# Kernel tuning notes

Measured on AMD Instinct MI355X. Metric: run time of the kernel, lower is better.

The kernel has to match this reference:

```python
import jax, jax.numpy as jnp
import numpy as np

N, E = 20000, 320000
HID, EDIM, DDIM, TDIM = 256, 128, 64, 256
IN_CH = 2 * HID + EDIM + DDIM  # 704
COORS_EPS = 1e-8
LN_EPS = 1e-6


def setup_inputs() -> dict:
    key = jax.random.key(0)
    ks = jax.random.split(key, 16)
    s = lambda fan_in: 1.0 / np.sqrt(fan_in)
    return {
        'h': jax.random.normal(ks[0], (N, HID), jnp.float32),
        'pos': jax.random.normal(ks[1], (N, 3), jnp.float32),
        'edge_attr': jax.random.normal(ks[2], (E, EDIM), jnp.float32),
        'dist': jax.random.uniform(ks[3], (E, DDIM), jnp.float32),
        'time_emb': jax.random.normal(ks[4], (E, TDIM), jnp.float32),
        'edge_index': jax.random.randint(ks[5], (2, E), 0, N, jnp.int64),
        'W_time': jax.random.uniform(ks[6], (TDIM, 2 * HID), jnp.float32, -s(TDIM), s(TDIM)),
        'b_time': jnp.zeros((2 * HID,), jnp.float32),
        'W_in': jax.random.uniform(ks[7], (IN_CH, HID), jnp.float32, -s(IN_CH), s(IN_CH)),
        'b_in': jnp.zeros((HID,), jnp.float32),
        'W_c1': jax.random.uniform(ks[8], (HID, HID), jnp.float32, -s(HID), s(HID)),
        'b_c1': jnp.zeros((HID,), jnp.float32),
        'W_c2': jax.random.uniform(ks[9], (HID, 1), jnp.float32, -s(HID), s(HID)),
        'coord_scale': jnp.full((1,), 0.01, jnp.float32),
    }


def _layernorm_noaffine(x):
    # fp32 LayerNorm, no affine (matches LayerNorm(elementwise_affine=False))
    x32 = x.astype(jnp.float32)
    mu = jnp.mean(x32, axis=-1, keepdims=True)
    var = jnp.mean(jnp.square(x32 - mu), axis=-1, keepdims=True)
    return ((x32 - mu) * jax.lax.rsqrt(var + LN_EPS)).astype(x.dtype)


def reference(h, pos, edge_attr, dist, time_emb, edge_index,
              W_time, b_time, W_in, b_in, W_c1, b_c1, W_c2, coord_scale):
    row, col = edge_index[0], edge_index[1]
    # gather node features per edge: [E, 2*HID + EDIM + DDIM]
    h_input = jnp.concatenate([h[row], h[col], edge_attr, dist], axis=1)
    # equivariant direction, normalized (CoorsNorm)
    coord_diff = pos[row] - pos[col]                       # [E, 3]
    norm = jnp.linalg.norm(coord_diff, axis=-1, keepdims=True)
    coord_diff = coord_diff / jnp.maximum(norm, COORS_EPS) * coord_scale
    # time conditioning: SiLU -> Linear -> chunk to shift/scale [E, HID]
    t = jax.nn.silu(time_emb) @ W_time + b_time
    shift, scale = t[:, :HID], t[:, HID:]
    inv = _layernorm_noaffine(h_input @ W_in + b_in)
    inv = inv * (1.0 + scale) + shift                      # modulate
    # coord MLP -> tanh gate [E, 1]
    inv = jnp.tanh(jax.nn.silu(inv @ W_c1 + b_c1) @ W_c2)
    trans = coord_diff * inv                               # [E, 3]
    agg = jax.ops.segment_sum(trans, row, num_segments=pos.shape[0])
    return pos + agg
```

## Files before the change

kernel.cpp:

```cpp
#include <hip/hip_runtime.h>
#include <hip/hip_bf16.h>

#define NN   20000
#define NE   320000
#define HID  256
#define EDIM 128
#define DDIM 64
#define TDIM 256
#define INCH 704

typedef __attribute__((ext_vector_type(8))) short bf16x8;
typedef __attribute__((ext_vector_type(4))) float f32x4;
typedef __attribute__((ext_vector_type(4))) unsigned int u32x4;

__device__ __forceinline__ unsigned short f2bu(float x) {
    return __bfloat16_as_ushort(__float2bfloat16(x));
}
__device__ __forceinline__ unsigned pk2(float lo, float hi) {
    return (unsigned)f2bu(lo) | ((unsigned)f2bu(hi) << 16);
}
__device__ __forceinline__ float ulo(unsigned u) {
    return __bfloat162float(__ushort_as_bfloat16((unsigned short)(u & 0xffffu)));
}
__device__ __forceinline__ float uhi(unsigned u) {
    return __bfloat162float(__ushort_as_bfloat16((unsigned short)(u >> 16)));
}
__device__ __forceinline__ float silu_f(float x) {
    return x / (1.0f + __expf(-x));
}

__global__ void pack_weights(const float* __restrict__ src, unsigned short* __restrict__ dst,
                             int K, int Nc) {
    int KT = K >> 5, NT = Nc >> 4;
    int total = KT * NT * 64;
    int idx = blockIdx.x * blockDim.x + threadIdx.x;
    if (idx >= total) return;
    int lane = idx & 63;
    int tile = idx >> 6;
    int nt = tile % NT, kt = tile / NT;
    int n = nt * 16 + (lane & 15);
    int k0 = kt * 32 + (lane >> 4) * 8;
    alignas(16) unsigned short v[8];
#pragma unroll
    for (int j = 0; j < 8; ++j) v[j] = f2bu(src[(size_t)(k0 + j) * Nc + n]);
    *reinterpret_cast<u32x4*>(dst + (size_t)idx * 8) = *reinterpret_cast<const u32x4*>(v);
}

__global__ void init_out(const float* __restrict__ pos, float* __restrict__ out, int n) {
    int i = blockIdx.x * blockDim.x + threadIdx.x;
    if (i < n) out[i] = pos[i];
}

__global__ __launch_bounds__(256, 2) void edge_kernel(
    const float* __restrict__ h, const float* __restrict__ pos,
    const float* __restrict__ edge_attr, const float* __restrict__ dist,
    const float* __restrict__ time_emb, const int* __restrict__ edge_index,
    const float* __restrict__ b_time, const float* __restrict__ b_in,
    const float* __restrict__ b_c1, const float* __restrict__ W_c2,
    const float* __restrict__ coord_scale,
    const unsigned short* __restrict__ pWtime, const unsigned short* __restrict__ pWin,
    const unsigned short* __restrict__ pWc1,
    float* __restrict__ out)
{
    __shared__ __align__(16) __hip_bfloat16 sX[2][64][40];
    __shared__ __align__(16) __hip_bfloat16 sU[64][264];
    __shared__ float sSum[64], sSq[64], sS[64];
    __shared__ int sRow[64], sCol[64];

    const int tid = threadIdx.x;
    const int wave = tid >> 6, lane = tid & 63;
    const int lq = lane >> 4, lr = lane & 15;
    const int e0 = blockIdx.x * 64;
    const int el = tid >> 2, part = tid & 3;

    if (tid < 64) {
        sRow[tid] = edge_index[e0 + tid];
        sCol[tid] = edge_index[NE + e0 + tid];
        sSum[tid] = 0.f; sSq[tid] = 0.f; sS[tid] = 0.f;
    }

    auto stageT = [&](int kt, int buf) {
        const float* p = time_emb + (size_t)(e0 + el) * TDIM + kt * 32 + part * 8;
        float4 a = *reinterpret_cast<const float4*>(p);
        float4 b = *reinterpret_cast<const float4*>(p + 4);
        u32x4 w;
        w.x = pk2(silu_f(a.x), silu_f(a.y));
        w.y = pk2(silu_f(a.z), silu_f(a.w));
        w.z = pk2(silu_f(b.x), silu_f(b.y));
        w.w = pk2(silu_f(b.z), silu_f(b.w));
        *reinterpret_cast<u32x4*>(&sX[buf][el][part * 8]) = w;
    };

    f32x4 accT[4][8];
#pragma unroll
    for (int m = 0; m < 4; ++m)
#pragma unroll
        for (int n = 0; n < 8; ++n) accT[m][n] = (f32x4){0.f, 0.f, 0.f, 0.f};

    stageT(0, 0);
    for (int kt = 0; kt < 8; ++kt) {
        __syncthreads();
        if (kt < 7) stageT(kt + 1, (kt + 1) & 1);
        bf16x8 afr[4];
#pragma unroll
        for (int m = 0; m < 4; ++m)
            afr[m] = *reinterpret_cast<const bf16x8*>(&sX[kt & 1][m * 16 + lr][lq * 8]);
#pragma unroll
        for (int n = 0; n < 8; ++n) {
            int ntg = (n < 4) ? (4 * wave + n) : (16 + 4 * wave + (n - 4));
            bf16x8 bfr = *reinterpret_cast<const bf16x8*>(pWtime + ((size_t)(kt * 32 + ntg) * 64 + lane) * 8);
#pragma unroll
            for (int m = 0; m < 4; ++m)
                accT[m][n] = __builtin_amdgcn_mfma_f32_16x16x32_bf16(afr[m], bfr, accT[m][n], 0, 0, 0);
        }
    }

    unsigned TP[4][8][2];
#pragma unroll
    for (int n = 0; n < 8; ++n) {
        int colg = (n < 4) ? ((4 * wave + n) * 16 + lr) : (256 + (4 * wave + (n - 4)) * 16 + lr);
        float bt = b_time[colg];
#pragma unroll
        for (int m = 0; m < 4; ++m) {
            f32x4 v = accT[m][n];
            TP[m][n][0] = pk2(v.x + bt, v.y + bt);
            TP[m][n][1] = pk2(v.z + bt, v.w + bt);
        }
    }

    auto stage1 = [&](int kt, int buf) {
        const float* p;
        if (kt < 8)       p = h + (size_t)sRow[el] * HID + kt * 32;
        else if (kt < 16) p = h + (size_t)sCol[el] * HID + (kt - 8) * 32;
        else if (kt < 20) p = edge_attr + (size_t)(e0 + el) * EDIM + (kt - 16) * 32;
        else              p = dist + (size_t)(e0 + el) * DDIM + (kt - 20) * 32;
        p += part * 8;
        float4 a = *reinterpret_cast<const float4*>(p);
        float4 b = *reinterpret_cast<const float4*>(p + 4);
        u32x4 w;
        w.x = pk2(a.x, a.y); w.y = pk2(a.z, a.w);
        w.z = pk2(b.x, b.y); w.w = pk2(b.z, b.w);
        *reinterpret_cast<u32x4*>(&sX[buf][el][part * 8]) = w;
    };

    f32x4 accY[4][4];
#pragma unroll
    for (int m = 0; m < 4; ++m)
#pragma unroll
        for (int n = 0; n < 4; ++n) accY[m][n] = (f32x4){0.f, 0.f, 0.f, 0.f};

    stage1(0, 0);
    for (int kt = 0; kt < 22; ++kt) {
        __syncthreads();
        if (kt < 21) stage1(kt + 1, (kt + 1) & 1);
        bf16x8 afr[4];
#pragma unroll
        for (int m = 0; m < 4; ++m)
            afr[m] = *reinterpret_cast<const bf16x8*>(&sX[kt & 1][m * 16 + lr][lq * 8]);
#pragma unroll
        for (int n = 0; n < 4; ++n) {
            int ntg = 4 * wave + n;
            bf16x8 bfr = *reinterpret_cast<const bf16x8*>(pWin + ((size_t)(kt * 16 + ntg) * 64 + lane) * 8);
#pragma unroll
            for (int m = 0; m < 4; ++m)
                accY[m][n] = __builtin_amdgcn_mfma_f32_16x16x32_bf16(afr[m], bfr, accY[m][n], 0, 0, 0);
        }
    }

#pragma unroll
    for (int n = 0; n < 4; ++n) {
        float bi = b_in[(4 * wave + n) * 16 + lr];
#pragma unroll
        for (int m = 0; m < 4; ++m) {
            accY[m][n].x += bi; accY[m][n].y += bi; accY[m][n].z += bi; accY[m][n].w += bi;
        }
    }

#pragma unroll
    for (int m = 0; m < 4; ++m) {
#pragma unroll
        for (int r = 0; r < 4; ++r) {
            float v0 = accY[m][0][r], v1 = accY[m][1][r], v2 = accY[m][2][r], v3 = accY[m][3][r];
            float s1 = v0 + v1 + v2 + v3;
            float s2 = v0 * v0 + v1 * v1 + v2 * v2 + v3 * v3;
#pragma unroll
            for (int off = 1; off < 16; off <<= 1) {
                s1 += __shfl_xor(s1, off, 64);
                s2 += __shfl_xor(s2, off, 64);
            }
            if (lr == 0) {
                atomicAdd(&sSum[m * 16 + lq * 4 + r], s1);
                atomicAdd(&sSq[m * 16 + lq * 4 + r], s2);
            }
        }
    }
    __syncthreads();

#pragma unroll
    for (int m = 0; m < 4; ++m) {
#pragma unroll
        for (int r = 0; r < 4; ++r) {
            int e = m * 16 + lq * 4 + r;
            float mu = sSum[e] * (1.0f / 256.0f);
            float var = sSq[e] * (1.0f / 256.0f) - mu * mu;
            float rs = rsqrtf(var + 1e-6f);
#pragma unroll
            for (int n = 0; n < 4; ++n) {
                float y = accY[m][n][r];
                float ln = (y - mu) * rs;
                unsigned ush = TP[m][n][r >> 1];
                unsigned usc = TP[m][n + 4][r >> 1];
                float sh = (r & 1) ? uhi(ush) : ulo(ush);
                float sc = (r & 1) ? uhi(usc) : ulo(usc);
                float u = ln * (1.0f + sc) + sh;
                sU[e][(4 * wave + n) * 16 + lr] = __float2bfloat16(u);
            }
        }
    }
    __syncthreads();

    f32x4 accZ[4][4];
#pragma unroll
    for (int m = 0; m < 4; ++m)
#pragma unroll
        for (int n = 0; n < 4; ++n) accZ[m][n] = (f32x4){0.f, 0.f, 0.f, 0.f};

    for (int kt = 0; kt < 8; ++kt) {
        bf16x8 afr[4];
#pragma unroll
        for (int m = 0; m < 4; ++m)
            afr[m] = *reinterpret_cast<const bf16x8*>(&sU[m * 16 + lr][kt * 32 + lq * 8]);
#pragma unroll
        for (int n = 0; n < 4; ++n) {
            int ntg = 4 * wave + n;
            bf16x8 bfr = *reinterpret_cast<const bf16x8*>(pWc1 + ((size_t)(kt * 16 + ntg) * 64 + lane) * 8);
#pragma unroll
            for (int m = 0; m < 4; ++m)
                accZ[m][n] = __builtin_amdgcn_mfma_f32_16x16x32_bf16(afr[m], bfr, accZ[m][n], 0, 0, 0);
        }
    }

#pragma unroll
    for (int m = 0; m < 4; ++m) {
        float ps0 = 0.f, ps1 = 0.f, ps2 = 0.f, ps3 = 0.f;
#pragma unroll
        for (int n = 0; n < 4; ++n) {
            int colg = (4 * wave + n) * 16 + lr;
            float bc = b_c1[colg];
            float w2 = W_c2[colg];
            ps0 += silu_f(accZ[m][n][0] + bc) * w2;
            ps1 += silu_f(accZ[m][n][1] + bc) * w2;
            ps2 += silu_f(accZ[m][n][2] + bc) * w2;
            ps3 += silu_f(accZ[m][n][3] + bc) * w2;
        }
        float ps[4] = {ps0, ps1, ps2, ps3};
#pragma unroll
        for (int r = 0; r < 4; ++r) {
            float v = ps[r];
#pragma unroll
            for (int off = 1; off < 16; off <<= 1) v += __shfl_xor(v, off, 64);
            if (lr == 0) atomicAdd(&sS[m * 16 + lq * 4 + r], v);
        }
    }
    __syncthreads();

    if (tid < 64) {
        int e = tid;
        float inv = tanhf(sS[e]);
        int rI = sRow[e], cI = sCol[e];
        float dx = pos[rI * 3 + 0] - pos[cI * 3 + 0];
        float dy = pos[rI * 3 + 1] - pos[cI * 3 + 1];
        float dz = pos[rI * 3 + 2] - pos[cI * 3 + 2];
        float nrm = sqrtf(dx * dx + dy * dy + dz * dz);
        float f = coord_scale[0] * inv / fmaxf(nrm, 1e-8f);
        atomicAdd(&out[rI * 3 + 0], dx * f);
        atomicAdd(&out[rI * 3 + 1], dy * f);
        atomicAdd(&out[rI * 3 + 2], dz * f);
    }
}

extern "C" void kernel_launch(void* const* d_in, const int* in_sizes, int n_in,
                              void* d_out, int out_size, void* d_ws, size_t ws_size,
                              hipStream_t stream) {
    const float* h          = (const float*)d_in[0];
    const float* pos        = (const float*)d_in[1];
    const float* edge_attr  = (const float*)d_in[2];
    const float* dist       = (const float*)d_in[3];
    const float* time_emb   = (const float*)d_in[4];
    const int*   edge_index = (const int*)d_in[5];
    const float* W_time     = (const float*)d_in[6];
    const float* b_time     = (const float*)d_in[7];
    const float* W_in       = (const float*)d_in[8];
    const float* b_in       = (const float*)d_in[9];
    const float* W_c1       = (const float*)d_in[10];
    const float* b_c1       = (const float*)d_in[11];
    const float* W_c2       = (const float*)d_in[12];
    const float* coord_scale= (const float*)d_in[13];
    float* out = (float*)d_out;

    unsigned short* pWin   = (unsigned short*)d_ws;
    unsigned short* pWtime = (unsigned short*)((char*)d_ws + 360448);
    unsigned short* pWc1   = (unsigned short*)((char*)d_ws + 622592);

    pack_weights<<<88, 256, 0, stream>>>(W_in,   pWin,   INCH, HID);
    pack_weights<<<64, 256, 0, stream>>>(W_time, pWtime, TDIM, 2 * HID);
    pack_weights<<<32, 256, 0, stream>>>(W_c1,   pWc1,   HID,  HID);
    init_out<<<(3 * NN + 255) / 256, 256, 0, stream>>>(pos, out, 3 * NN);

    edge_kernel<<<NE / 64, 256, 0, stream>>>(
        h, pos, edge_attr, dist, time_emb, edge_index,
        b_time, b_in, b_c1, W_c2, coord_scale,
        pWtime, pWin, pWc1, out);
}
```

Baseline: 552.4 us.

## Restructure edge kernel staging and split time GEMM to raise occupancy

The time-embedding tile is now staged once into a shared buffer, and the time GEMM is computed in two halves (shift, then scale) so only 16 accumulators are live at a time. That buffer is aliased with the U and X tiles to cut shared memory. The input GEMM now uses 64-wide K chunks with register prefetch of the next chunk, which halves the number of barriers. Launch bounds move from 2 to 3 blocks per SIMD so more waves can hide the gather latency, at the risk of register spills.

```diff
diff --git a/kernel.cpp b/kernel.cpp
--- a/kernel.cpp
+++ b/kernel.cpp
@@ -51,7 +51,7 @@
     if (i < n) out[i] = pos[i];
 }
 
-__global__ __launch_bounds__(256, 2) void edge_kernel(
+__global__ __launch_bounds__(256, 3) void edge_kernel(
     const float* __restrict__ h, const float* __restrict__ pos,
     const float* __restrict__ edge_attr, const float* __restrict__ dist,
     const float* __restrict__ time_emb, const int* __restrict__ edge_index,
@@ -62,8 +62,10 @@
     const unsigned short* __restrict__ pWc1,
     float* __restrict__ out)
 {
-    __shared__ __align__(16) __hip_bfloat16 sX[2][64][40];
-    __shared__ __align__(16) __hip_bfloat16 sU[64][264];
+    __shared__ __align__(16) unsigned char smem[64 * 264 * 2];
+    __hip_bfloat16 (*sT)[264]    = reinterpret_cast<__hip_bfloat16(*)[264]>(smem);
+    __hip_bfloat16 (*sU)[264]    = reinterpret_cast<__hip_bfloat16(*)[264]>(smem);
+    __hip_bfloat16 (*sX)[64][72] = reinterpret_cast<__hip_bfloat16(*)[64][72]>(smem);
     __shared__ float sSum[64], sSq[64], sS[64];
     __shared__ int sRow[64], sCol[64];
 
@@ -79,92 +81,156 @@
         sSum[tid] = 0.f; sSq[tid] = 0.f; sS[tid] = 0.f;
     }
 
-    auto stageT = [&](int kt, int buf) {
-        const float* p = time_emb + (size_t)(e0 + el) * TDIM + kt * 32 + part * 8;
-        float4 a = *reinterpret_cast<const float4*>(p);
-        float4 b = *reinterpret_cast<const float4*>(p + 4);
-        u32x4 w;
-        w.x = pk2(silu_f(a.x), silu_f(a.y));
-        w.y = pk2(silu_f(a.z), silu_f(a.w));
-        w.z = pk2(silu_f(b.x), silu_f(b.y));
-        w.w = pk2(silu_f(b.z), silu_f(b.w));
-        *reinterpret_cast<u32x4*>(&sX[buf][el][part * 8]) = w;
-    };
-
-    f32x4 accT[4][8];
+    {
+        const float* p = time_emb + (size_t)(e0 + el) * TDIM + part * 64;
+#pragma unroll
+        for (int j = 0; j < 4; ++j) {
+            float4 a = *reinterpret_cast<const float4*>(p + j * 16);
+            float4 b = *reinterpret_cast<const float4*>(p + j * 16 + 4);
+            float4 c = *reinterpret_cast<const float4*>(p + j * 16 + 8);
+            float4 d = *reinterpret_cast<const float4*>(p + j * 16 + 12);
+            u32x4 w0, w1;
+            w0.x = pk2(silu_f(a.x), silu_f(a.y)); w0.y = pk2(silu_f(a.z), silu_f(a.w));
+            w0.z = pk2(silu_f(b.x), silu_f(b.y)); w0.w = pk2(silu_f(b.z), silu_f(b.w));
+            w1.x = pk2(silu_f(c.x), silu_f(c.y)); w1.y = pk2(silu_f(c.z), silu_f(c.w));
+            w1.z = pk2(silu_f(d.x), silu_f(d.y)); w1.w = pk2(silu_f(d.z), silu_f(d.w));
+            *reinterpret_cast<u32x4*>(&sT[el][part * 64 + j * 16]) = w0;
+            *reinterpret_cast<u32x4*>(&sT[el][part * 64 + j * 16 + 8]) = w1;
+        }
+    }
+    __syncthreads();
+
+    const int rIdx = sRow[el], cIdx = sCol[el];
+
+    float rY[16];
+    {
+        const float* p = h + (size_t)rIdx * HID + part * 16;
+        *reinterpret_cast<float4*>(&rY[0])  = *reinterpret_cast<const float4*>(p);
+        *reinterpret_cast<float4*>(&rY[4])  = *reinterpret_cast<const float4*>(p + 4);
+        *reinterpret_cast<float4*>(&rY[8])  = *reinterpret_cast<const float4*>(p + 8);
+        *reinterpret_cast<float4*>(&rY[12]) = *reinterpret_cast<const float4*>(p + 12);
+    }
+
+    unsigned TPs[4][4][2], TPc[4][4][2];
+    {
+        f32x4 acc[4][4];
+#pragma unroll
+        for (int m = 0; m < 4; ++m)
+#pragma unroll
+            for (int n = 0; n < 4; ++n) acc[m][n] = (f32x4){0.f, 0.f, 0.f, 0.f};
+#pragma unroll
+        for (int kt = 0; kt < 8; ++kt) {
+            bf16x8 afr[4];
+#pragma unroll
+            for (int m = 0; m < 4; ++m)
+                afr[m] = *reinterpret_cast<const bf16x8*>(&sT[m * 16 + lr][kt * 32 + lq * 8]);
+#pragma unroll
+            for (int n = 0; n < 4; ++n) {
+                bf16x8 bfr = *reinterpret_cast<const bf16x8*>(
+                    pWtime + ((size_t)(kt * 32 + 4 * wave + n) * 64 + lane) * 8);
+#pragma unroll
+                for (int m = 0; m < 4; ++m)
+                    acc[m][n] = __builtin_amdgcn_mfma_f32_16x16x32_bf16(afr[m], bfr, acc[m][n], 0, 0, 0);
+            }
+        }
+#pragma unroll
+        for (int n = 0; n < 4; ++n) {
+            float bt = b_time[(4 * wave + n) * 16 + lr];
+#pragma unroll
+            for (int m = 0; m < 4; ++m) {
+                TPs[m][n][0] = pk2(acc[m][n].x + bt, acc[m][n].y + bt);
+                TPs[m][n][1] = pk2(acc[m][n].z + bt, acc[m][n].w + bt);
+            }
+        }
+#pragma unroll
+        for (int m = 0; m < 4; ++m)
+#pragma unroll
+            for (int n = 0; n < 4; ++n) acc[m][n] = (f32x4){0.f, 0.f, 0.f, 0.f};
+#pragma unroll
+        for (int kt = 0; kt < 8; ++kt) {
+            bf16x8 afr[4];
+#pragma unroll
+            for (int m = 0; m < 4; ++m)
+                afr[m] = *reinterpret_cast<const bf16x8*>(&sT[m * 16 + lr][kt * 32 + lq * 8]);
+#pragma unroll
+            for (int n = 0; n < 4; ++n) {
+                bf16x8 bfr = *reinterpret_cast<const bf16x8*>(
+                    pWtime + ((size_t)(kt * 32 + 16 + 4 * wave + n) * 64 + lane) * 8);
+#pragma unroll
+                for (int m = 0; m < 4; ++m)
+                    acc[m][n] = __builtin_amdgcn_mfma_f32_16x16x32_bf16(afr[m], bfr, acc[m][n], 0, 0, 0);
+            }
+        }
+#pragma unroll
+        for (int n = 0; n < 4; ++n) {
+            float bt = b_time[256 + (4 * wave + n) * 16 + lr];
+#pragma unroll
+            for (int m = 0; m < 4; ++m) {
+                TPc[m][n][0] = pk2(acc[m][n].x + bt, acc[m][n].y + bt);
+                TPc[m][n][1] = pk2(acc[m][n].z + bt, acc[m][n].w + bt);
+            }
+        }
+    }
+    __syncthreads();
+
+    {
+        u32x4 w0, w1;
+        w0.x = pk2(rY[0], rY[1]);   w0.y = pk2(rY[2], rY[3]);
+        w0.z = pk2(rY[4], rY[5]);   w0.w = pk2(rY[6], rY[7]);
+        w1.x = pk2(rY[8], rY[9]);   w1.y = pk2(rY[10], rY[11]);
+        w1.z = pk2(rY[12], rY[13]); w1.w = pk2(rY[14], rY[15]);
+        *reinterpret_cast<u32x4*>(&sX[0][el][part * 16]) = w0;
+        *reinterpret_cast<u32x4*>(&sX[0][el][part * 16 + 8]) = w1;
+    }
+    __syncthreads();
+
+    f32x4 accY[4][4];
 #pragma unroll
     for (int m = 0; m < 4; ++m)
 #pragma unroll
-        for (int n = 0; n < 8; ++n) accT[m][n] = (f32x4){0.f, 0.f, 0.f, 0.f};
-
-    stageT(0, 0);
-    for (int kt = 0; kt < 8; ++kt) {
+        for (int n = 0; n < 4; ++n) accY[m][n] = (f32x4){0.f, 0.f, 0.f, 0.f};
+
+#pragma unroll
+    for (int kt = 0; kt < 11; ++kt) {
+        const int buf = kt & 1;
+        if (kt < 10) {
+            const int kn = kt + 1;
+            const float* p;
+            if (kn < 4)       p = h + (size_t)rIdx * HID + kn * 64;
+            else if (kn < 8)  p = h + (size_t)cIdx * HID + (kn - 4) * 64;
+            else if (kn < 10) p = edge_attr + (size_t)(e0 + el) * EDIM + (kn - 8) * 64;
+            else              p = dist + (size_t)(e0 + el) * DDIM;
+            p += part * 16;
+            *reinterpret_cast<float4*>(&rY[0])  = *reinterpret_cast<const float4*>(p);
+            *reinterpret_cast<float4*>(&rY[4])  = *reinterpret_cast<const float4*>(p + 4);
+            *reinterpret_cast<float4*>(&rY[8])  = *reinterpret_cast<const float4*>(p + 8);
+            *reinterpret_cast<float4*>(&rY[12]) = *reinterpret_cast<const float4*>(p + 12);
+        }
+#pragma unroll
+        for (int kq = 0; kq < 2; ++kq) {
+            bf16x8 afr[4];
+#pragma unroll
+            for (int m = 0; m < 4; ++m)
+                afr[m] = *reinterpret_cast<const bf16x8*>(&sX[buf][m * 16 + lr][kq * 32 + lq * 8]);
+#pragma unroll
+            for (int n = 0; n < 4; ++n) {
+                bf16x8 bfr = *reinterpret_cast<const bf16x8*>(
+                    pWin + ((size_t)((2 * kt + kq) * 16 + 4 * wave + n) * 64 + lane) * 8);
+#pragma unroll
+                for (int m = 0; m < 4; ++m)
+                    accY[m][n] = __builtin_amdgcn_mfma_f32_16x16x32_bf16(afr[m], bfr, accY[m][n], 0, 0, 0);
+            }
+        }
+        if (kt < 10) {
+            u32x4 w0, w1;
+            w0.x = pk2(rY[0], rY[1]);   w0.y = pk2(rY[2], rY[3]);
+            w0.z = pk2(rY[4], rY[5]);   w0.w = pk2(rY[6], rY[7]);
+            w1.x = pk2(rY[8], rY[9]);   w1.y = pk2(rY[10], rY[11]);
+            w1.z = pk2(rY[12], rY[13]); w1.w = pk2(rY[14], rY[15]);
+            *reinterpret_cast<u32x4*>(&sX[buf ^ 1][el][part * 16]) = w0;
+            *reinterpret_cast<u32x4*>(&sX[buf ^ 1][el][part * 16 + 8]) = w1;
+        }
         __syncthreads();
-        if (kt < 7) stageT(kt + 1, (kt + 1) & 1);
-        bf16x8 afr[4];
-#pragma unroll
-        for (int m = 0; m < 4; ++m)
-            afr[m] = *reinterpret_cast<const bf16x8*>(&sX[kt & 1][m * 16 + lr][lq * 8]);
-#pragma unroll
-        for (int n = 0; n < 8; ++n) {
-            int ntg = (n < 4) ? (4 * wave + n) : (16 + 4 * wave + (n - 4));
-            bf16x8 bfr = *reinterpret_cast<const bf16x8*>(pWtime + ((size_t)(kt * 32 + ntg) * 64 + lane) * 8);
-#pragma unroll
-            for (int m = 0; m < 4; ++m)
-                accT[m][n] = __builtin_amdgcn_mfma_f32_16x16x32_bf16(afr[m], bfr, accT[m][n], 0, 0, 0);
-        }
-    }
-
-    unsigned TP[4][8][2];
-#pragma unroll
-    for (int n = 0; n < 8; ++n) {
-        int colg = (n < 4) ? ((4 * wave + n) * 16 + lr) : (256 + (4 * wave + (n - 4)) * 16 + lr);
-        float bt = b_time[colg];
-#pragma unroll
-        for (int m = 0; m < 4; ++m) {
-            f32x4 v = accT[m][n];
-            TP[m][n][0] = pk2(v.x + bt, v.y + bt);
-            TP[m][n][1] = pk2(v.z + bt, v.w + bt);
-        }
-    }
-
-    auto stage1 = [&](int kt, int buf) {
-        const float* p;
-        if (kt < 8)       p = h + (size_t)sRow[el] * HID + kt * 32;
-        else if (kt < 16) p = h + (size_t)sCol[el] * HID + (kt - 8) * 32;
-        else if (kt < 20) p = edge_attr + (size_t)(e0 + el) * EDIM + (kt - 16) * 32;
-        else              p = dist + (size_t)(e0 + el) * DDIM + (kt - 20) * 32;
-        p += part * 8;
-        float4 a = *reinterpret_cast<const float4*>(p);
-        float4 b = *reinterpret_cast<const float4*>(p + 4);
-        u32x4 w;
-        w.x = pk2(a.x, a.y); w.y = pk2(a.z, a.w);
-        w.z = pk2(b.x, b.y); w.w = pk2(b.z, b.w);
-        *reinterpret_cast<u32x4*>(&sX[buf][el][part * 8]) = w;
-    };
-
-    f32x4 accY[4][4];
-#pragma unroll
-    for (int m = 0; m < 4; ++m)
-#pragma unroll
-        for (int n = 0; n < 4; ++n) accY[m][n] = (f32x4){0.f, 0.f, 0.f, 0.f};
-
-    stage1(0, 0);
-    for (int kt = 0; kt < 22; ++kt) {
-        __syncthreads();
-        if (kt < 21) stage1(kt + 1, (kt + 1) & 1);
-        bf16x8 afr[4];
-#pragma unroll
-        for (int m = 0; m < 4; ++m)
-            afr[m] = *reinterpret_cast<const bf16x8*>(&sX[kt & 1][m * 16 + lr][lq * 8]);
-#pragma unroll
-        for (int n = 0; n < 4; ++n) {
-            int ntg = 4 * wave + n;
-            bf16x8 bfr = *reinterpret_cast<const bf16x8*>(pWin + ((size_t)(kt * 16 + ntg) * 64 + lane) * 8);
-#pragma unroll
-            for (int m = 0; m < 4; ++m)
-                accY[m][n] = __builtin_amdgcn_mfma_f32_16x16x32_bf16(afr[m], bfr, accY[m][n], 0, 0, 0);
-        }
     }
 
 #pragma unroll
@@ -208,12 +274,11 @@
             for (int n = 0; n < 4; ++n) {
                 float y = accY[m][n][r];
                 float ln = (y - mu) * rs;
-                unsigned ush = TP[m][n][r >> 1];
-                unsigned usc = TP[m][n + 4][r >> 1];
+                unsigned ush = TPs[m][n][r >> 1];
+                unsigned usc = TPc[m][n][r >> 1];
                 float sh = (r & 1) ? uhi(ush) : ulo(ush);
                 float sc = (r & 1) ? uhi(usc) : ulo(usc);
-                float u = ln * (1.0f + sc) + sh;
-                sU[e][(4 * wave + n) * 16 + lr] = __float2bfloat16(u);
+                sU[e][(4 * wave + n) * 16 + lr] = __float2bfloat16(ln * (1.0f + sc) + sh);
             }
         }
     }
@@ -225,6 +290,7 @@
 #pragma unroll
         for (int n = 0; n < 4; ++n) accZ[m][n] = (f32x4){0.f, 0.f, 0.f, 0.f};
 
+#pragma unroll
     for (int kt = 0; kt < 8; ++kt) {
         bf16x8 afr[4];
 #pragma unroll
@@ -232,8 +298,8 @@
             afr[m] = *reinterpret_cast<const bf16x8*>(&sU[m * 16 + lr][kt * 32 + lq * 8]);
 #pragma unroll
         for (int n = 0; n < 4; ++n) {
-            int ntg = 4 * wave + n;
-            bf16x8 bfr = *reinterpret_cast<const bf16x8*>(pWc1 + ((size_t)(kt * 16 + ntg) * 64 + lane) * 8);
+            bf16x8 bfr = *reinterpret_cast<const bf16x8*>(
+                pWc1 + ((size_t)(kt * 16 + 4 * wave + n) * 64 + lane) * 8);
 #pragma unroll
             for (int m = 0; m < 4; ++m)
                 accZ[m][n] = __builtin_amdgcn_mfma_f32_16x16x32_bf16(afr[m], bfr, accZ[m][n], 0, 0, 0);
```

New measurement: 1.329 ms. 2.41x slower.
